# Performance work log

Measured on AMD Instinct MI355X. Metric: run time of the kernel, lower is better.

Reference implementation:

```python
import jax, jax.numpy as jnp
import numpy as np
from jax import lax

V_PATCH_NUMS = (1, 2, 3, 4, 5, 6, 8, 10, 13, 16)
SHARE_K = 4
RESI = 0.5  # abs(quant_resi)


def _area_matrix(pn, H):
    # F.interpolate(mode='area') == adaptive_avg_pool2d: uniform mean over [floor, ceil) window
    W = np.zeros((pn, H), np.float32)
    for i in range(pn):
        s = int(np.floor(i * H / pn)); e = int(np.ceil((i + 1) * H / pn))
        W[i, s:e] = 1.0 / (e - s)
    return W


def _cubic(x, a=-0.75):
    x = abs(x)
    if x <= 1.0:
        return (a + 2) * x**3 - (a + 3) * x**2 + 1
    if x < 2.0:
        return a * x**3 - 5 * a * x**2 + 8 * a * x - 4 * a
    return 0.0


def _bicubic_matrix(out, inp):
    # torch bicubic, align_corners=False, a=-0.75, border-clamped (separable 1D matrix)
    W = np.zeros((out, inp), np.float32)
    for i in range(out):
        src = (i + 0.5) * inp / out - 0.5
        i0 = int(np.floor(src)); t = src - i0
        for k in range(-1, 3):
            j = min(max(i0 + k, 0), inp - 1)
            W[i, j] += _cubic(k - t)
    return W


def _phi_select(si, SN, K=SHARE_K):
    ticks = np.linspace(1 / 3 / K, 1 - 1 / 3 / K, K) if K == 4 else np.linspace(1 / 2 / K, 1 - 1 / 2 / K, K)
    return int(np.argmin(np.abs(ticks - si / (SN - 1))))


def _phi(h, w, b):
    # Phi: h*(1-r) + conv3x3(h)*r
    y = lax.conv_general_dilated(h, w, (1, 1), 'SAME',
                                 dimension_numbers=('NCHW', 'OIHW', 'NCHW'))
    y = y + b[None, :, None, None]
    return h * (1.0 - RESI) + y * RESI


def reference(f, embedding, phi_w, phi_b):
    # Multi-scale residual vector quantization (VectorQuantizer2 hot path).
    # f: [B, C, 16, 16] latent; embedding: [V, C]; phi_w: [K, C, C, 3, 3]; phi_b: [K, C]
    B, C, H, Wd = f.shape
    SN = len(V_PATCH_NUMS)
    e2 = jnp.sum(embedding**2, axis=1)  # [V]
    f_hat = jnp.zeros_like(f)
    f_rest = f
    for si, pn in enumerate(V_PATCH_NUMS):
        if si != SN - 1:
            A = jnp.asarray(_area_matrix(pn, H))
            z = jnp.einsum('ph,bchw,qw->bcpq', A, f_rest, A)  # area downsample to pn x pn
        else:
            z = f_rest
        zf = z.transpose(0, 2, 3, 1).reshape(-1, C)  # [B*pn*pn, C]
        # squared-distance cdist + argmin codebook lookup
        d = jnp.sum(zf**2, axis=1, keepdims=True) - 2.0 * (zf @ embedding.T) + e2[None, :]
        idx = jnp.argmin(d, axis=1)  # [B*pn*pn]
        h = embedding[idx].reshape(B, pn, pn, C).transpose(0, 3, 1, 2)  # gather -> [B,C,pn,pn]
        if si != SN - 1:
            U = jnp.asarray(_bicubic_matrix(H, pn))
            h = jnp.einsum('hp,bcpq,wq->bchw', U, h, U)  # bicubic upsample to H x W
        k = _phi_select(si, SN)
        h = _phi(h, phi_w[k], phi_b[k])  # partially-shared Phi residual refinement
        f_hat = f_hat + h
        f_rest = f_rest - h
    return f_hat


def setup_inputs() -> dict:
    key = jax.random.key(0)
    k1, k2, k3 = jax.random.split(key, 3)
    f = jax.random.normal(k1, (64, 32, 16, 16), dtype=jnp.float32)
    embedding = jax.random.normal(k2, (4096, 32), dtype=jnp.float32)
    phi_w = jax.random.normal(k3, (4, 32, 32, 3, 3), dtype=jnp.float32) * 0.05
    phi_b = jnp.zeros((4, 32), dtype=jnp.float32)
    return {"f": f, "embedding": embedding, "phi_w": phi_w, "phi_b": phi_b}
```

## Files before the change

kernel.cpp:

```cpp
#include <hip/hip_runtime.h>
#include <cmath>


#define BB 64
#define CC 32
#define HH 16
#define VV 4096
#define NTOT (BB*CC*HH*HH)

typedef __attribute__((ext_vector_type(8))) short bf16x8;
typedef __attribute__((ext_vector_type(4))) float f32x4;

__device__ __forceinline__ double cubicw(double x) {
    x = fabs(x);
    const double a = -0.75;
    if (x <= 1.0) return ((a + 2.0) * x - (a + 3.0)) * x * x + 1.0;
    if (x < 2.0)  return (((a * x - 5.0 * a) * x + 8.0 * a) * x - 4.0 * a);
    return 0.0;
}

__device__ __forceinline__ unsigned int ordf(float d) {
    unsigned int b = __float_as_uint(d);
    return (b & 0x80000000u) ? ~b : (b | 0x80000000u);
}

__device__ __forceinline__ short f2bf(float x) {
    unsigned u = __float_as_uint(x);
    unsigned r = (u + 0x7fffu + ((u >> 16) & 1u)) >> 16;
    return (short)r;
}
__device__ __forceinline__ float bf2f(short h) {
    return __uint_as_float(((unsigned)(unsigned short)h) << 16);
}

__global__ void init_k(const float* __restrict__ f, const float* __restrict__ E,
                       float* __restrict__ f_rest, float* __restrict__ f_hat,
                       float* __restrict__ e2, float* __restrict__ z,
                       unsigned short* __restrict__ est) {
    int i = blockIdx.x * 256 + threadIdx.x;
    if (i < NTOT) { f_rest[i] = f[i]; f_hat[i] = 0.f; }
    if (i < VV) {
        float s = 0.f;
        int tile = i >> 4, n = i & 15;
        #pragma unroll
        for (int c = 0; c < CC; ++c) {
            float x = E[i * CC + c];
            s += x * x;
            if (est) {
                short h = f2bf(x); float rm = x - bf2f(h);
                short m = f2bf(rm); float rl = rm - bf2f(m);
                short l = f2bf(rl);
                int idx = tile * 1536 + (n * 4 + (c >> 3)) * 8 + (c & 7);
                est[idx]        = (unsigned short)h;
                est[idx + 512]  = (unsigned short)m;
                est[idx + 1024] = (unsigned short)l;
            }
        }
        e2[i] = s;
    }
    if (i < BB * CC) {
        const float* src = f + (size_t)i * (HH * HH);
        float s = 0.f;
        for (int j = 0; j < HH * HH; ++j) s += src[j];
        z[i] = s * (1.0f / 256.0f);
    }
}

__global__ __launch_bounds__(256, 4) void argsmall_k(const float* __restrict__ z,
        const float* __restrict__ E, const float* __restrict__ e2,
        unsigned long long* __restrict__ bestk, int M, int G, int gsz) {
    const int t = threadIdx.x;
    int m = blockIdx.x * 64 + (t & 63);
    int w = __builtin_amdgcn_readfirstlane(t >> 6);
    int wg = blockIdx.y * 4 + w;
    int v0 = wg * gsz;
    float zr[CC]; float z2 = 0.f;
    const float4* zp = (const float4*)(z + (size_t)m * CC);
    #pragma unroll
    for (int c4 = 0; c4 < 8; ++c4) {
        float4 v = zp[c4];
        zr[c4*4+0] = v.x; zr[c4*4+1] = v.y; zr[c4*4+2] = v.z; zr[c4*4+3] = v.w;
        z2 += v.x*v.x + v.y*v.y + v.z*v.z + v.w*v.w;
    }
    const float* e = E + (size_t)v0 * CC;
    float best = 3.4e38f; int bv = v0;
    for (int v = v0; v < v0 + gsz; v += 2, e += 2 * CC) {
        float a0 = 0.f, a1 = 0.f, b0 = 0.f, b1 = 0.f;
        #pragma unroll
        for (int c = 0; c < CC; c += 2) {
            a0 = fmaf(zr[c],   e[c],      a0);
            a1 = fmaf(zr[c+1], e[c+1],    a1);
            b0 = fmaf(zr[c],   e[CC+c],   b0);
            b1 = fmaf(zr[c+1], e[CC+c+1], b1);
        }
        float dA = fmaf(-2.f, a0 + a1, z2 + e2[v]);
        float dB = fmaf(-2.f, b0 + b1, z2 + e2[v+1]);
        if (dA < best) { best = dA; bv = v; }
        if (dB < best) { best = dB; bv = v + 1; }
    }
    bestk[(size_t)m * G + wg] = ((unsigned long long)ordf(best) << 32) |
                                (unsigned long long)(unsigned int)bv;
}

__global__ __launch_bounds__(256, 4) void argmf_k(const unsigned short* __restrict__ zs,
        const unsigned short* __restrict__ est, const float* __restrict__ e2,
        unsigned long long* __restrict__ bestk, int M, int G, int gsz) {
    const int t = threadIdx.x;
    const int g = blockIdx.y;
    const int v0 = g * gsz;
    const int lane = t & 63;
    const int w = t >> 6;
    const int n = lane & 15, kq = lane >> 4;

    int tb[2]; bf16x8 ah[2], am[2], al[2];
    #pragma unroll
    for (int pt = 0; pt < 2; ++pt) {
        int tb0 = blockIdx.x * 128 + w * 32 + pt * 16;
        if (tb0 > M - 16) tb0 = M - 16;
        tb[pt] = tb0;
        const unsigned short* zp = zs + (size_t)(tb0 + n) * 96 + kq * 8;
        ah[pt] = *(const bf16x8*)(zp);
        am[pt] = *(const bf16x8*)(zp + 32);
        al[pt] = *(const bf16x8*)(zp + 64);
    }

    float bd[2][4]; int bc[2][4];
    #pragma unroll
    for (int pt = 0; pt < 2; ++pt)
        #pragma unroll
        for (int r = 0; r < 4; ++r) { bd[pt][r] = 3.4e38f; bc[pt][r] = 0; }

    const int nct = gsz >> 4;
    const unsigned short* ep = est + (size_t)(v0 >> 4) * 1536 +
                               (size_t)(n * 4 + kq) * 8;
    const float* e2p = e2 + v0 + n;
    for (int ct = 0; ct < nct; ++ct, ep += 1536, e2p += 16) {
        bf16x8 eh = *(const bf16x8*)(ep);
        bf16x8 em = *(const bf16x8*)(ep + 512);
        bf16x8 el = *(const bf16x8*)(ep + 1024);
        float e2c = *e2p;
        #pragma unroll
        for (int pt = 0; pt < 2; ++pt) {
            f32x4 Ca = {0.f, 0.f, 0.f, 0.f};
            f32x4 Cb = {e2c, e2c, e2c, e2c};
            Ca = __builtin_amdgcn_mfma_f32_16x16x32_bf16(ah[pt], eh, Ca, 0, 0, 0);
            Cb = __builtin_amdgcn_mfma_f32_16x16x32_bf16(am[pt], eh, Cb, 0, 0, 0);
            Ca = __builtin_amdgcn_mfma_f32_16x16x32_bf16(ah[pt], em, Ca, 0, 0, 0);
            Cb = __builtin_amdgcn_mfma_f32_16x16x32_bf16(al[pt], eh, Cb, 0, 0, 0);
            Ca = __builtin_amdgcn_mfma_f32_16x16x32_bf16(ah[pt], el, Ca, 0, 0, 0);
            Cb = __builtin_amdgcn_mfma_f32_16x16x32_bf16(am[pt], em, Cb, 0, 0, 0);
            #pragma unroll
            for (int r = 0; r < 4; ++r) {
                float d = Ca[r] + Cb[r];
                if (d < bd[pt][r]) { bd[pt][r] = d; bc[pt][r] = ct; }
            }
        }
    }
    #pragma unroll
    for (int pt = 0; pt < 2; ++pt) {
        #pragma unroll
        for (int r = 0; r < 4; ++r) {
            int v = v0 + bc[pt][r] * 16 + n;
            unsigned long long k = ((unsigned long long)ordf(bd[pt][r]) << 32) |
                                   (unsigned long long)(unsigned int)v;
            #pragma unroll
            for (int msk = 1; msk < 16; msk <<= 1) {
                unsigned long long o = __shfl_xor(k, msk);
                if (o < k) k = o;
            }
            if (n == 0)
                bestk[(size_t)(tb[pt] + kq * 4 + r) * G + g] = k;
        }
    }
}

__global__ __launch_bounds__(256, 4) void argbig_k(const float* __restrict__ z,
        const float* __restrict__ E, const float* __restrict__ e2,
        unsigned long long* __restrict__ bestk, int M, int G, int gsz) {
    __shared__ float s_e[128 * CC];
    __shared__ float s_e2[128];
    const int T = gridDim.x * 256;
    const int g = blockIdx.y;
    const int v0 = g * gsz;
    {
        const float4* src = (const float4*)(E + (size_t)v0 * CC);
        float4* dst = (float4*)s_e;
        for (int i = threadIdx.x; i < gsz * 8; i += 256) dst[i] = src[i];
        if (threadIdx.x < gsz) s_e2[threadIdx.x] = e2[v0 + threadIdx.x];
    }
    int   mm[2];
    bool  act[2];
    float zr[2][CC];
    float z2[2];
    #pragma unroll
    for (int pt = 0; pt < 2; ++pt) {
        int m0 = blockIdx.x * 256 + threadIdx.x + pt * T;
        act[pt] = (m0 < M);
        int m = act[pt] ? m0 : M - 1;
        mm[pt] = m;
        const float4* zp = (const float4*)(z + (size_t)m * CC);
        float zz = 0.f;
        #pragma unroll
        for (int c4 = 0; c4 < 8; ++c4) {
            float4 v = zp[c4];
            zr[pt][c4*4+0] = v.x; zr[pt][c4*4+1] = v.y;
            zr[pt][c4*4+2] = v.z; zr[pt][c4*4+3] = v.w;
            zz += v.x*v.x + v.y*v.y + v.z*v.z + v.w*v.w;
        }
        z2[pt] = zz;
    }
    __syncthreads();
    float best[2]; int bv[2];
    #pragma unroll
    for (int pt = 0; pt < 2; ++pt) { best[pt] = 3.4e38f; bv[pt] = v0; }
    const float4* ev = (const float4*)s_e;
    for (int vi = 0; vi < gsz; ++vi, ev += 8) {
        float4 e0 = ev[0], e1 = ev[1], e2v = ev[2], e3 = ev[3];
        float4 e4 = ev[4], e5 = ev[5], e6v = ev[6], e7 = ev[7];
        float ef[CC] = {e0.x,e0.y,e0.z,e0.w, e1.x,e1.y,e1.z,e1.w,
                        e2v.x,e2v.y,e2v.z,e2v.w, e3.x,e3.y,e3.z,e3.w,
                        e4.x,e4.y,e4.z,e4.w, e5.x,e5.y,e5.z,e5.w,
                        e6v.x,e6v.y,e6v.z,e6v.w, e7.x,e7.y,e7.z,e7.w};
        float a0 = 0.f, a1 = 0.f, b0 = 0.f, b1 = 0.f;
        #pragma unroll
        for (int c = 0; c < CC; c += 2) {
            a0 = fmaf(zr[0][c],   ef[c],   a0);
            a1 = fmaf(zr[0][c+1], ef[c+1], a1);
            b0 = fmaf(zr[1][c],   ef[c],   b0);
            b1 = fmaf(zr[1][c+1], ef[c+1], b1);
        }
        float e2c = s_e2[vi];
        float dA = fmaf(-2.f, a0 + a1, z2[0] + e2c);
        float dB = fmaf(-2.f, b0 + b1, z2[1] + e2c);
        int v = v0 + vi;
        if (dA < best[0]) { best[0] = dA; bv[0] = v; }
        if (dB < best[1]) { best[1] = dB; bv[1] = v; }
    }
    #pragma unroll
    for (int pt = 0; pt < 2; ++pt)
        if (act[pt])
            bestk[(size_t)mm[pt] * G + g] =
                ((unsigned long long)ordf(best[pt]) << 32) |
                (unsigned long long)(unsigned int)bv[pt];
}

__global__ __launch_bounds__(512) void fuse_k(const unsigned long long* __restrict__ bestk,
                      const float* __restrict__ E,
                      const float* __restrict__ pw, const float* __restrict__ pb,
                      float* __restrict__ f_hat, float* __restrict__ f_rest,
                      float* __restrict__ z_next, unsigned short* __restrict__ zsn,
                      int pn, int G, int TPP, int kphi, int pnn) {
    __shared__ float s_buf[CC * 18 * 20];
    __shared__ float s_pw[CC * 3 * 4 * 8];
    __shared__ float s_part[3 * 128 * 20];
    __shared__ int   s_idx[256];
    __shared__ float s_w[HH][4];
    __shared__ int   s_j[HH][4];
    __shared__ unsigned long long s_red[512];
    const int t   = threadIdx.x;
    const int cog = blockIdx.x;
    const int b   = blockIdx.y;
    const int P   = pn * pn;
    const int half = t >> 8;
    const int tl   = t & 255;

    {
        int p = t / TPP, sub = t - p * TPP;
        unsigned long long bk = ~0ull;
        if (p < P) {
            const unsigned long long* kp = bestk + (size_t)(b * P + p) * G;
            for (int gg = sub; gg < G; gg += TPP) {
                unsigned long long o = kp[gg];
                if (o < bk) bk = o;
            }
        }
        s_red[t] = bk;
        __syncthreads();
        for (int s = TPP >> 1; s > 0; s >>= 1) {
            if ((sub < s) && p < P) {
                unsigned long long o = s_red[t + s];
                if (o < s_red[t]) s_red[t] = o;
            }
            __syncthreads();
        }
        if (t < P) s_idx[t] = (int)(unsigned int)(s_red[t * TPP] & 0xffffffffull);
    }
    if (t < HH) {
        double src = (t + 0.5) * (double)pn / 16.0 - 0.5;
        double fi = floor(src); int i0 = (int)fi; double tt = src - fi;
        #pragma unroll
        for (int k = 0; k < 4; ++k) {
            int j = i0 - 1 + k; j = j < 0 ? 0 : (j > pn - 1 ? pn - 1 : j);
            s_j[t][k] = j;
            s_w[t][k] = (float)cubicw((double)(k - 1) - tt);
        }
    }
    {
        const float* src = pw + ((size_t)(kphi * CC + cog * 8)) * CC * 9;
        for (int i = t; i < 8 * CC * 9; i += 512) {
            int l  = i / (CC * 9);
            int r  = i - l * (CC * 9);
            int ci = r / 9; int kk = r - ci * 9;
            int kh = kk / 3; int kw = kk - kh * 3;
            int cp = l >> 1, ce = l & 1;
            s_pw[ci * 96 + kh * 32 + cp * 8 + ce * 4 + kw] = src[i];
        }
    }
    __syncthreads();

    if (tl < HH * pn) {
        int h = tl / pn, q = tl % pn;
        int cbase = half * 16;
        float acc[16];
        #pragma unroll
        for (int c = 0; c < 16; ++c) acc[c] = 0.f;
        #pragma unroll
        for (int k = 0; k < 4; ++k) {
            float wv = s_w[h][k];
            if (wv == 0.0f) continue;
            int row = s_idx[s_j[h][k] * pn + q];
            const float4* er = (const float4*)(E + (size_t)row * CC + cbase);
            #pragma unroll
            for (int c4 = 0; c4 < 4; ++c4) {
                float4 e4 = er[c4];
                acc[c4*4+0] = fmaf(wv, e4.x, acc[c4*4+0]);
                acc[c4*4+1] = fmaf(wv, e4.y, acc[c4*4+1]);
                acc[c4*4+2] = fmaf(wv, e4.z, acc[c4*4+2]);
                acc[c4*4+3] = fmaf(wv, e4.w, acc[c4*4+3]);
            }
        }
        #pragma unroll
        for (int c = 0; c < 16; ++c)
            s_buf[((cbase + c) * HH + h) * pn + q] = acc[c];
    }
    __syncthreads();

    {
        int h = tl >> 4, w = tl & 15;
        int cbase = half * 16;
        float acc[16];
        #pragma unroll
        for (int c = 0; c < 16; ++c) acc[c] = 0.f;
        #pragma unroll
        for (int k = 0; k < 4; ++k) {
            float wh = s_w[w][k];
            int j = s_j[w][k];
            #pragma unroll
            for (int c = 0; c < 16; ++c)
                acc[c] = fmaf(wh, s_buf[((cbase + c) * HH + h) * pn + j], acc[c]);
        }
        __syncthreads();
        #pragma unroll
        for (int c = 0; c < 16; ++c)
            s_buf[((cbase + c) * 18 + h + 1) * 20 + w + 1] = acc[c];
        if (w == 0) {
            #pragma unroll
            for (int c = 0; c < 16; ++c) s_buf[((cbase + c) * 18 + h + 1) * 20] = 0.f;
        }
        if (w >= 13) {
            #pragma unroll
            for (int c = 0; c < 16; ++c) s_buf[((cbase + c) * 18 + h + 1) * 20 + w + 4] = 0.f;
        }
        if (h == 0) {
            #pragma unroll
            for (int c = 0; c < 16; ++c) {
                s_buf[((cbase + c) * 18) * 20 + w] = 0.f;
                if (w < 4) s_buf[((cbase + c) * 18) * 20 + 16 + w] = 0.f;
            }
        }
        if (h == 15) {
            #pragma unroll
            for (int c = 0; c < 16; ++c) {
                s_buf[((cbase + c) * 18 + 17) * 20 + w] = 0.f;
                if (w < 4) s_buf[((cbase + c) * 18 + 17) * 20 + 16 + w] = 0.f;
            }
        }
    }
    __syncthreads();

    const int cp  = tl >> 6;
    const int q   = (tl >> 5) & 1;
    const int s   = tl & 31;
    const int h   = s >> 1;
    const int w0  = (s & 1) * 8;
    const int wid = half * 2 + q;
    const int pos = cp * 32 + s;
    float accE[8], accO[8];
    #pragma unroll
    for (int o = 0; o < 8; ++o) { accE[o] = 0.f; accO[o] = 0.f; }
    const int ci0 = wid * 8;
    for (int ci = ci0; ci < ci0 + 8; ++ci) {
        const float* wrow = &s_pw[ci * 96 + cp * 8];
        #pragma unroll
        for (int kk = 0; kk < 3; ++kk) {
            int kh = kk + q; kh = (kh >= 3) ? kh - 3 : kh;
            const float4* xr = (const float4*)&s_buf[(ci * 18 + h + kh) * 20 + w0];
            float4 a0 = xr[0], a1 = xr[1], a2 = xr[2];
            float xf[12] = {a0.x, a0.y, a0.z, a0.w, a1.x, a1.y, a1.z, a1.w,
                            a2.x, a2.y, a2.z, a2.w};
            const float4* wp = (const float4*)(wrow + kh * 32);
            float4 wA = wp[0];
            float4 wB = wp[1];
            #pragma unroll
            for (int o = 0; o < 8; ++o) {
                accE[o] += xf[o] * wA.x + xf[o+1] * wA.y + xf[o+2] * wA.z;
                accO[o] += xf[o] * wB.x + xf[o+1] * wB.y + xf[o+2] * wB.z;
            }
        }
    }
    if (wid != 0) {
        float* dst = &s_part[((wid - 1) * 128 + pos) * 20];
        *(float4*)(dst +  0) = make_float4(accE[0], accE[1], accE[2], accE[3]);
        *(float4*)(dst +  4) = make_float4(accE[4], accE[5], accE[6], accE[7]);
        *(float4*)(dst +  8) = make_float4(accO[0], accO[1], accO[2], accO[3]);
        *(float4*)(dst + 12) = make_float4(accO[4], accO[5], accO[6], accO[7]);
    }
    __syncthreads();

    float4 rE0, rE1, rO0, rO1;
    if (wid == 0) {
        #pragma unroll
        for (int g2 = 0; g2 < 3; ++g2) {
            const float* sp = &s_part[(g2 * 128 + pos) * 20];
            float4 p0 = *(const float4*)(sp + 0), p1 = *(const float4*)(sp + 4);
            float4 p2 = *(const float4*)(sp + 8), p3 = *(const float4*)(sp + 12);
            accE[0] += p0.x; accE[1] += p0.y; accE[2] += p0.z; accE[3] += p0.w;
            accE[4] += p1.x; accE[5] += p1.y; accE[6] += p1.z; accE[7] += p1.w;
            accO[0] += p2.x; accO[1] += p2.y; accO[2] += p2.z; accO[3] += p2.w;
            accO[4] += p3.x; accO[5] += p3.y; accO[6] += p3.z; accO[7] += p3.w;
        }
        float biasE = pb[kphi * CC + cog * 8 + cp * 2];
        float biasO = pb[kphi * CC + cog * 8 + cp * 2 + 1];
        #pragma unroll
        for (int o = 0; o < 8; ++o) { accE[o] += biasE; accO[o] += biasO; }
        #pragma unroll
        for (int c = 0; c < 2; ++c) {
            const float* acc = c ? accO : accE;
            int co = cog * 8 + cp * 2 + c;
            float hf[8];
            #pragma unroll
            for (int o = 0; o < 8; ++o) {
                float hv = s_buf[(co * 18 + h + 1) * 20 + w0 + o + 1];
                hf[o] = 0.5f * hv + 0.5f * acc[o];
            }
            size_t base = ((size_t)(b * CC + co) * HH + h) * HH + w0;
            float4* fh = (float4*)(f_hat + base);
            float4* fr = (float4*)(f_rest + base);
            float4 v0 = fh[0], v1 = fh[1];
            v0.x += hf[0]; v0.y += hf[1]; v0.z += hf[2]; v0.w += hf[3];
            v1.x += hf[4]; v1.y += hf[5]; v1.z += hf[6]; v1.w += hf[7];
            fh[0] = v0; fh[1] = v1;
            float4 r0 = fr[0], r1 = fr[1];
            r0.x -= hf[0]; r0.y -= hf[1]; r0.z -= hf[2]; r0.w -= hf[3];
            r1.x -= hf[4]; r1.y -= hf[5]; r1.z -= hf[6]; r1.w -= hf[7];
            fr[0] = r0; fr[1] = r1;
            if (c) { rO0 = r0; rO1 = r1; } else { rE0 = r0; rE1 = r1; }
        }
    }

    if (pnn > 0) {
        __syncthreads();
        float* fn = s_buf;
        if (wid == 0) {
            #pragma unroll
            for (int c = 0; c < 2; ++c) {
                int cl = cp * 2 + c;
                float* d = &fn[(cl * HH + h) * HH + w0];
                float4 r0 = c ? rO0 : rE0, r1 = c ? rO1 : rE1;
                d[0] = r0.x; d[1] = r0.y; d[2] = r0.z; d[3] = r0.w;
                d[4] = r1.x; d[5] = r1.y; d[6] = r1.z; d[7] = r1.w;
            }
        }
        __syncthreads();
        int P2 = pnn * pnn;
        for (int i = t; i < P2 * 8; i += 512) {
            int cl = i & 7, pq = i >> 3;
            int q2 = pq % pnn, p2 = pq / pnn;
            int sp = (p2 * HH) / pnn, ep = ((p2 + 1) * HH + pnn - 1) / pnn;
            int sq = (q2 * HH) / pnn, eq = ((q2 + 1) * HH + pnn - 1) / pnn;
            float wgt = 1.0f / ((float)(ep - sp) * (float)(eq - sq));
            float sum = 0.f;
            for (int h2 = sp; h2 < ep; ++h2)
                for (int w2 = sq; w2 < eq; ++w2)
                    sum += fn[(cl * HH + h2) * HH + w2];
            float v = sum * wgt;
            int c = cog * 8 + cl;
            if (zsn) {
                float tv = -2.0f * v;
                size_t baz = (size_t)(b * P2 + pq) * 96 + c;
                unsigned short hh = (unsigned short)f2bf(tv);
                float rm = tv - bf2f((short)hh);
                unsigned short mm2 = (unsigned short)f2bf(rm);
                float rl = rm - bf2f((short)mm2);
                unsigned short ll = (unsigned short)f2bf(rl);
                zsn[baz] = hh; zsn[baz + 32] = mm2; zsn[baz + 64] = ll;
            } else {
                z_next[((size_t)(b * P2 + pq)) * CC + c] = v;
            }
        }
    }
}

extern "C" void kernel_launch(void* const* d_in, const int* in_sizes, int n_in,
                              void* d_out, int out_size, void* d_ws, size_t ws_size,
                              hipStream_t stream) {
    const float* f  = (const float*)d_in[0];
    const float* E  = (const float*)d_in[1];
    const float* pw = (const float*)d_in[2];
    const float* pb = (const float*)d_in[3];
    float* out = (float*)d_out;

    const size_t need_base = (size_t)(NTOT + VV) * 4 + (size_t)524288 * 8 +
                             (size_t)524288 * 4;
    const size_t need_mf = need_base + (size_t)VV * 96 * 2 +
                           (size_t)16384 * 96 * 2;
    const bool use_mf = (ws_size >= need_mf);

    float* wsf    = (float*)d_ws;
    float* f_rest = wsf;
    float* e2     = wsf + (size_t)NTOT;
    unsigned long long* bestk = (unsigned long long*)(e2 + VV);
    float* z      = (float*)(bestk + 524288);
    unsigned short* est = use_mf ? (unsigned short*)(z + 524288) : (unsigned short*)0;
    unsigned short* zs  = use_mf ? (est + (size_t)VV * 96) : (unsigned short*)0;

    int phik[10];
    {
        double start = 1.0 / 3.0 / 4.0;
        double stop  = 1.0 - 1.0 / 3.0 / 4.0;
        double step  = (stop - start) / 3.0;
        double ticks[4];
        for (int i = 0; i < 4; ++i) ticks[i] = (double)i * step + start;
        ticks[3] = stop;
        for (int si = 0; si < 10; ++si) {
            double s = (double)si / 9.0;
            int bk = 0; double bd = fabs(ticks[0] - s);
            for (int tq = 1; tq < 4; ++tq) {
                double d2 = fabs(ticks[tq] - s);
                if (d2 < bd) { bd = d2; bk = tq; }
            }
            phik[si] = bk;
        }
    }

    static const int pns[10]  = {1, 2, 3, 4, 5, 6, 8, 10, 13, 16};
    static const int grpS[10] = {256, 128, 64, 32, 32, 16, 0, 0, 0, 0};
    static const int grpF[10] = {0, 0, 0, 0, 0, 0, 128, 64, 32, 32};
    static const int grpM[10] = {0, 0, 0, 32, 32, 32, 16, 16, 8, 8};

    init_k<<<(NTOT + 255) / 256, 256, 0, stream>>>(f, E, f_rest, out, e2, z, est);

    for (int si = 0; si < 10; ++si) {
        int pn = pns[si];
        int P = pn * pn;
        int M = BB * P;
        int G, TPP;
        bool small_path = use_mf ? (pn <= 3) : (pn <= 6);
        if (small_path) {
            int grp = grpS[si];
            G = grp * 4;
            int gsz = VV / G;
            argsmall_k<<<dim3(P, grp), 256, 0, stream>>>(z, E, e2, bestk, M, G, gsz);
        } else if (use_mf) {
            G = grpM[si];
            int gsz = VV / G;
            int bx = (M + 127) / 128;
            argmf_k<<<dim3(bx, G), 256, 0, stream>>>(zs, est, e2, bestk, M, G, gsz);
        } else {
            G = grpF[si];
            int gsz = VV / G;
            int bx = (M + 511) / 512;
            argbig_k<<<dim3(bx, G), 256, 0, stream>>>(z, E, e2, bestk, M, G, gsz);
        }
        TPP = 1;
        while (TPP * 2 * P <= 512) TPP *= 2;
        int pnn = (si < 9) ? pns[si + 1] : 0;
        unsigned short* zsn = (pnn >= 4 && use_mf) ? zs : (unsigned short*)0;
        fuse_k<<<dim3(4, BB), 512, 0, stream>>>(bestk, E, pw, pb,
                                                out, f_rest, z, zsn,
                                                pn, G, TPP, phik[si], pnn);
    }
}
```

Baseline: 392.0 us.

## Prefetch codebook tiles, use wave shuffles for argmin reduce, restage upsample in LDS

The distance kernel now loads the next codebook tile into registers while the MFMAs on the current one run (software prefetch). In the fuse kernel, the LDS tree reduction over candidate keys, which used a barrier per step, is replaced by wave-level xor shuffles and a short final pass per point. The intermediate bicubic row pass is stored position-major in a separate scratch buffer with float4 accesses. That buffer also holds the conv partial sums, so one intra-loop barrier goes away. The cost is more registers for the prefetch and a larger total shared-memory footprint, which could lower occupancy.

```diff
diff --git a/kernel.cpp b/kernel.cpp
--- a/kernel.cpp
+++ b/kernel.cpp
@@ -134,21 +134,29 @@
     const unsigned short* ep = est + (size_t)(v0 >> 4) * 1536 +
                                (size_t)(n * 4 + kq) * 8;
     const float* e2p = e2 + v0 + n;
-    for (int ct = 0; ct < nct; ++ct, ep += 1536, e2p += 16) {
-        bf16x8 eh = *(const bf16x8*)(ep);
-        bf16x8 em = *(const bf16x8*)(ep + 512);
-        bf16x8 el = *(const bf16x8*)(ep + 1024);
-        float e2c = *e2p;
+    bf16x8 eh = *(const bf16x8*)(ep);
+    bf16x8 em = *(const bf16x8*)(ep + 512);
+    bf16x8 el = *(const bf16x8*)(ep + 1024);
+    float e2c = *e2p;
+    for (int ct = 0; ct < nct; ++ct) {
+        bf16x8 ceh = eh, cem = em, cel = el; float ce2 = e2c;
+        if (ct + 1 < nct) {
+            ep += 1536; e2p += 16;
+            eh = *(const bf16x8*)(ep);
+            em = *(const bf16x8*)(ep + 512);
+            el = *(const bf16x8*)(ep + 1024);
+            e2c = *e2p;
+        }
         #pragma unroll
         for (int pt = 0; pt < 2; ++pt) {
             f32x4 Ca = {0.f, 0.f, 0.f, 0.f};
-            f32x4 Cb = {e2c, e2c, e2c, e2c};
-            Ca = __builtin_amdgcn_mfma_f32_16x16x32_bf16(ah[pt], eh, Ca, 0, 0, 0);
-            Cb = __builtin_amdgcn_mfma_f32_16x16x32_bf16(am[pt], eh, Cb, 0, 0, 0);
-            Ca = __builtin_amdgcn_mfma_f32_16x16x32_bf16(ah[pt], em, Ca, 0, 0, 0);
-            Cb = __builtin_amdgcn_mfma_f32_16x16x32_bf16(al[pt], eh, Cb, 0, 0, 0);
-            Ca = __builtin_amdgcn_mfma_f32_16x16x32_bf16(ah[pt], el, Ca, 0, 0, 0);
-            Cb = __builtin_amdgcn_mfma_f32_16x16x32_bf16(am[pt], em, Cb, 0, 0, 0);
+            f32x4 Cb = {ce2, ce2, ce2, ce2};
+            Ca = __builtin_amdgcn_mfma_f32_16x16x32_bf16(ah[pt], ceh, Ca, 0, 0, 0);
+            Cb = __builtin_amdgcn_mfma_f32_16x16x32_bf16(am[pt], ceh, Cb, 0, 0, 0);
+            Ca = __builtin_amdgcn_mfma_f32_16x16x32_bf16(ah[pt], cem, Ca, 0, 0, 0);
+            Cb = __builtin_amdgcn_mfma_f32_16x16x32_bf16(al[pt], ceh, Cb, 0, 0, 0);
+            Ca = __builtin_amdgcn_mfma_f32_16x16x32_bf16(ah[pt], cel, Ca, 0, 0, 0);
+            Cb = __builtin_amdgcn_mfma_f32_16x16x32_bf16(am[pt], cem, Cb, 0, 0, 0);
             #pragma unroll
             for (int r = 0; r < 4; ++r) {
                 float d = Ca[r] + Cb[r];
@@ -251,12 +259,12 @@
                       float* __restrict__ z_next, unsigned short* __restrict__ zsn,
                       int pn, int G, int TPP, int kphi, int pnn) {
     __shared__ float s_buf[CC * 18 * 20];
+    __shared__ float s_scratch[256 * 36];
     __shared__ float s_pw[CC * 3 * 4 * 8];
-    __shared__ float s_part[3 * 128 * 20];
     __shared__ int   s_idx[256];
     __shared__ float s_w[HH][4];
     __shared__ int   s_j[HH][4];
-    __shared__ unsigned long long s_red[512];
+    __shared__ unsigned long long s_red[256];
     const int t   = threadIdx.x;
     const int cog = blockIdx.x;
     const int b   = blockIdx.y;
@@ -274,16 +282,19 @@
                 if (o < bk) bk = o;
             }
         }
-        s_red[t] = bk;
-        __syncthreads();
-        for (int s = TPP >> 1; s > 0; s >>= 1) {
-            if ((sub < s) && p < P) {
-                unsigned long long o = s_red[t + s];
-                if (o < s_red[t]) s_red[t] = o;
-            }
-            __syncthreads();
-        }
-        if (t < P) s_idx[t] = (int)(unsigned int)(s_red[t * TPP] & 0xffffffffull);
+        int bfly = TPP > 64 ? 64 : TPP;
+        for (int msk = 1; msk < bfly; msk <<= 1) {
+            unsigned long long o = __shfl_xor(bk, msk);
+            if (o < bk) bk = o;
+        }
+        if (p < P) {
+            if (TPP <= 64) {
+                if (sub == 0) s_red[p] = bk;
+            } else {
+                int K = TPP >> 6;
+                if ((sub & 63) == 0) s_red[p * K + (sub >> 6)] = bk;
+            }
+        }
     }
     if (t < HH) {
         double src = (t + 0.5) * (double)pn / 16.0 - 0.5;
@@ -307,6 +318,18 @@
         }
     }
     __syncthreads();
+    if (t < P) {
+        unsigned long long r = s_red[(TPP <= 64) ? t : t * (TPP >> 6)];
+        if (TPP > 64) {
+            int K = TPP >> 6;
+            for (int j2 = 1; j2 < K; ++j2) {
+                unsigned long long o = s_red[t * K + j2];
+                if (o < r) r = o;
+            }
+        }
+        s_idx[t] = (int)(unsigned int)(r & 0xffffffffull);
+    }
+    __syncthreads();
 
     if (tl < HH * pn) {
         int h = tl / pn, q = tl % pn;
@@ -329,9 +352,11 @@
                 acc[c4*4+3] = fmaf(wv, e4.w, acc[c4*4+3]);
             }
         }
-        #pragma unroll
-        for (int c = 0; c < 16; ++c)
-            s_buf[((cbase + c) * HH + h) * pn + q] = acc[c];
+        float* dst = &s_scratch[(h * pn + q) * 36 + cbase];
+        *(float4*)(dst + 0)  = make_float4(acc[0],  acc[1],  acc[2],  acc[3]);
+        *(float4*)(dst + 4)  = make_float4(acc[4],  acc[5],  acc[6],  acc[7]);
+        *(float4*)(dst + 8)  = make_float4(acc[8],  acc[9],  acc[10], acc[11]);
+        *(float4*)(dst + 12) = make_float4(acc[12], acc[13], acc[14], acc[15]);
     }
     __syncthreads();
 
@@ -345,11 +370,17 @@
         for (int k = 0; k < 4; ++k) {
             float wh = s_w[w][k];
             int j = s_j[w][k];
-            #pragma unroll
-            for (int c = 0; c < 16; ++c)
-                acc[c] = fmaf(wh, s_buf[((cbase + c) * HH + h) * pn + j], acc[c]);
-        }
-        __syncthreads();
+            const float4* sp4 = (const float4*)&s_scratch[(h * pn + j) * 36 + cbase];
+            float4 v0 = sp4[0], v1 = sp4[1], v2 = sp4[2], v3 = sp4[3];
+            acc[0]  = fmaf(wh, v0.x, acc[0]);  acc[1]  = fmaf(wh, v0.y, acc[1]);
+            acc[2]  = fmaf(wh, v0.z, acc[2]);  acc[3]  = fmaf(wh, v0.w, acc[3]);
+            acc[4]  = fmaf(wh, v1.x, acc[4]);  acc[5]  = fmaf(wh, v1.y, acc[5]);
+            acc[6]  = fmaf(wh, v1.z, acc[6]);  acc[7]  = fmaf(wh, v1.w, acc[7]);
+            acc[8]  = fmaf(wh, v2.x, acc[8]);  acc[9]  = fmaf(wh, v2.y, acc[9]);
+            acc[10] = fmaf(wh, v2.z, acc[10]); acc[11] = fmaf(wh, v2.w, acc[11]);
+            acc[12] = fmaf(wh, v3.x, acc[12]); acc[13] = fmaf(wh, v3.y, acc[13]);
+            acc[14] = fmaf(wh, v3.z, acc[14]); acc[15] = fmaf(wh, v3.w, acc[15]);
+        }
         #pragma unroll
         for (int c = 0; c < 16; ++c)
             s_buf[((cbase + c) * 18 + h + 1) * 20 + w + 1] = acc[c];
@@ -409,7 +440,7 @@
         }
     }
     if (wid != 0) {
-        float* dst = &s_part[((wid - 1) * 128 + pos) * 20];
+        float* dst = &s_scratch[((wid - 1) * 128 + pos) * 20];
         *(float4*)(dst +  0) = make_float4(accE[0], accE[1], accE[2], accE[3]);
         *(float4*)(dst +  4) = make_float4(accE[4], accE[5], accE[6], accE[7]);
         *(float4*)(dst +  8) = make_float4(accO[0], accO[1], accO[2], accO[3]);
@@ -421,7 +452,7 @@
     if (wid == 0) {
         #pragma unroll
         for (int g2 = 0; g2 < 3; ++g2) {
-            const float* sp = &s_part[(g2 * 128 + pos) * 20];
+            const float* sp = &s_scratch[(g2 * 128 + pos) * 20];
             float4 p0 = *(const float4*)(sp + 0), p1 = *(const float4*)(sp + 4);
             float4 p2 = *(const float4*)(sp + 8), p3 = *(const float4*)(sp + 12);
             accE[0] += p0.x; accE[1] += p0.y; accE[2] += p0.z; accE[3] += p0.w;
```

Measured after the change: 374.5 us. 1.05x faster.
